# Kernel optimization log

Measured on AMD Instinct MI355X. Metric: run time of the kernel, lower is better.

Reference implementation:

```python
import jax, jax.numpy as jnp
import numpy as np

MARGIN = 1.0
BIG = 1e4  # larger than any cosine distance (max 2.0)

def setup_inputs() -> dict:
    key = jax.random.key(0)
    k1, k2 = jax.random.split(key)
    embeddings = jax.random.normal(k1, (4096, 512), dtype=jnp.float32)
    labels = jax.random.randint(k2, (4096,), 0, 512, dtype=jnp.int64)
    return {"embeddings": embeddings, "labels": labels}

def reference(embeddings, labels):
    b = embeddings.shape[0]
    # L2-normalize rows (torch F.normalize uses eps=1e-12 clamp on norm)
    norms = jnp.linalg.norm(embeddings, axis=1, keepdims=True)
    emb_n = embeddings / jnp.maximum(norms, 1e-12)
    sim = emb_n @ emb_n.T                      # [b, b]
    dist = jnp.maximum(1.0 - sim, 0.0)         # cosine distance, clamped at 0

    same = labels[:, None] == labels[None, :]  # [b, b]
    eye = jnp.eye(b, dtype=bool)
    pos_mask = same & ~eye
    neg_mask = ~same

    # batch-hard mining: row-wise masked max over positives, min over negatives
    hardest_pos = jnp.max(jnp.where(pos_mask, dist, 0.0), axis=1)   # dist >= 0 so 0 is neutral for max
    hardest_neg = jnp.min(jnp.where(neg_mask, dist, BIG), axis=1)

    valid = jnp.any(pos_mask, axis=1) & jnp.any(neg_mask, axis=1)
    per_row = jax.nn.relu(hardest_pos - hardest_neg + MARGIN)
    loss_sum = jnp.sum(jnp.where(valid, per_row, 0.0))
    num_valid = jnp.sum(valid)
    return loss_sum / jnp.maximum(num_valid, 1).astype(loss_sum.dtype)
```

## Files before the change

### kernel.cpp

```cpp
#include <hip/hip_runtime.h>
#include <hip/hip_bf16.h>

#define BATCH 4096
#define DIM   512
#define NLBL  512
#define BIGF  1e4f
#define MARGIN 1.0f

#define BM 128
#define BK 32
#define NT (BATCH/BM)
#define NPAIR (NT*(NT+1)/2)
#define KITERS (DIM/BK)

#define PANEL_E 4096
#define TILE_E  65536

using f32x4  = __attribute__((ext_vector_type(4))) float;
using bf16x8 = __attribute__((ext_vector_type(8))) short;

struct PairTab { unsigned char bi[NPAIR]; unsigned char bj[NPAIR]; };
constexpr PairTab make_tab() {
    PairTab t{};
    int idx = 0;
    for (int BI = 0; BI < 8; ++BI)
        for (int BJ = BI; BJ < 8; ++BJ)
            for (int ii = 0; ii < 4; ++ii)
                for (int jj = 0; jj < 4; ++jj) {
                    int i = BI * 4 + ii, j = BJ * 4 + jj;
                    if (i <= j) {
                        t.bi[idx] = (unsigned char)i;
                        t.bj[idx] = (unsigned char)j;
                        ++idx;
                    }
                }
    return t;
}
__device__ constexpr PairTab PT = make_tab();

__device__ __forceinline__ unsigned short f2bf(float x) {
    __hip_bfloat16 h = __float2bfloat16(x);
    return *reinterpret_cast<unsigned short*>(&h);
}

#define GLOAD16(gp, lp) \
    __builtin_amdgcn_global_load_lds((const __attribute__((address_space(1))) void*)(gp), \
                                     (__attribute__((address_space(3))) void*)(lp), 16, 0, 0)

__global__ __launch_bounds__(256) void normalize_k(const float* __restrict__ emb,
                                                   unsigned short* __restrict__ HiT,
                                                   unsigned* __restrict__ hp,
                                                   unsigned* __restrict__ hn) {
    int wave = threadIdx.x >> 6;
    int lane = threadIdx.x & 63;
    int row  = blockIdx.x * 4 + wave;
    const float4* src = (const float4*)(emb + (size_t)row * DIM);
    float4 v0 = src[lane * 2];
    float4 v1 = src[lane * 2 + 1];
    float ss = v0.x*v0.x + v0.y*v0.y + v0.z*v0.z + v0.w*v0.w
             + v1.x*v1.x + v1.y*v1.y + v1.z*v1.z + v1.w*v1.w;
    #pragma unroll
    for (int off = 1; off < 64; off <<= 1) ss += __shfl_xor(ss, off);
    float scale = 1.0f / fmaxf(sqrtf(ss), 1e-12f);
    bf16x8 o;
    o[0] = (short)f2bf(v0.x * scale);
    o[1] = (short)f2bf(v0.y * scale);
    o[2] = (short)f2bf(v0.z * scale);
    o[3] = (short)f2bf(v0.w * scale);
    o[4] = (short)f2bf(v1.x * scale);
    o[5] = (short)f2bf(v1.y * scale);
    o[6] = (short)f2bf(v1.z * scale);
    o[7] = (short)f2bf(v1.w * scale);
    size_t off = (size_t)(row >> 7) * TILE_E + (size_t)(lane >> 2) * PANEL_E
               + (size_t)(row & 127) * 32 + (lane & 3) * 8;
    *(bf16x8*)(HiT + off) = o;
    if (lane == 0) {
        hp[row] = 0u;
        hn[row] = __float_as_uint(BIGF);
    }
}

__global__ __launch_bounds__(256, 4) void mine_k(const unsigned short* __restrict__ HiT,
                                                 const int* __restrict__ lab,
                                                 unsigned* __restrict__ hp,
                                                 unsigned* __restrict__ hn) {
    __shared__ __attribute__((aligned(16))) unsigned short As[2][BM * BK];
    __shared__ __attribute__((aligned(16))) unsigned short Bs[2][BM * BK];
    __shared__ float rowp[2][BM], rown[2][BM], colp[2][BM], coln[2][BM];

    int orig = (int)blockIdx.x;
    int p = (orig & 7) * (NPAIR / 8) + (orig >> 3);
    const int bi = PT.bi[p];
    const int bj = PT.bj[p];
    const int i0 = bi * BM;
    const int j0 = bj * BM;

    const int tid  = threadIdx.x;
    const int w    = tid >> 6;
    const int lane = tid & 63;
    const int wr   = w >> 1;
    const int wc   = w & 1;
    const int l15  = lane & 15;
    const int lhi  = lane >> 4;

    f32x4 acc[4][4] = {};
    const char* HiB = (const char*)HiT;

    auto STAGE = [&](int buf, int t) {
        const size_t pa = ((size_t)bi * 16 + t) * (PANEL_E * 2);
        const size_t pb = ((size_t)bj * 16 + t) * (PANEL_E * 2);
        const int rrel = lane >> 2;
        #pragma unroll
        for (int q = 0; q < 2; ++q) {
            const int R   = w * 32 + q * 16 + rrel;
            const int sc  = (lane & 3) ^ ((R >> 1) & 3);
            const int soff = (w * 2048 + q * 1024) + rrel * 64 + (sc << 4);
            GLOAD16(HiB + pa + soff, (char*)As[buf] + (w * 32 + q * 16) * 64);
            GLOAD16(HiB + pb + soff, (char*)Bs[buf] + (w * 32 + q * 16) * 64);
        }
    };
    auto COMPUTE = [&](int buf) {
        bf16x8 a[4], b[4];
        #pragma unroll
        for (int m = 0; m < 4; ++m) {
            int row = wr * 64 + m * 16 + l15;
            int cp  = lhi ^ ((row >> 1) & 3);
            a[m] = *(const bf16x8*)((const char*)As[buf] + row * 64 + (cp << 4));
        }
        #pragma unroll
        for (int n = 0; n < 4; ++n) {
            int row = wc * 64 + n * 16 + l15;
            int cp  = lhi ^ ((row >> 1) & 3);
            b[n] = *(const bf16x8*)((const char*)Bs[buf] + row * 64 + (cp << 4));
        }
        #pragma unroll
        for (int m = 0; m < 4; ++m)
            #pragma unroll
            for (int n = 0; n < 4; ++n)
                acc[m][n] = __builtin_amdgcn_mfma_f32_16x16x32_bf16(a[m], b[n], acc[m][n], 0, 0, 0);
    };

    STAGE(0, 0);
    STAGE(1, 1);
    #pragma unroll
    for (int t = 0; t < KITERS; ++t) {
        const int cur = t & 1;
        if (t < KITERS - 1) {
            asm volatile("s_waitcnt vmcnt(4)" ::: "memory");
        } else {
            asm volatile("s_waitcnt vmcnt(0)" ::: "memory");
        }
        __builtin_amdgcn_sched_barrier(0);
        __builtin_amdgcn_s_barrier();
        COMPUTE(cur);
        __builtin_amdgcn_sched_barrier(0);
        __builtin_amdgcn_s_barrier();
        if (t + 2 < KITERS) STAGE(cur, t + 2);
    }

    int lj[4];
    #pragma unroll
    for (int n = 0; n < 4; ++n) lj[n] = lab[j0 + wc * 64 + n * 16 + l15];
    int li[16];
    #pragma unroll
    for (int m = 0; m < 4; ++m)
        #pragma unroll
        for (int r = 0; r < 4; ++r)
            li[m * 4 + r] = lab[i0 + wr * 64 + m * 16 + lhi * 4 + r];

    #pragma unroll
    for (int m = 0; m < 4; ++m) {
        #pragma unroll
        for (int r = 0; r < 4; ++r) {
            int i   = i0 + wr * 64 + m * 16 + lhi * 4 + r;
            int lir = li[m * 4 + r];
            float pm = 0.0f, nm = BIGF;
            #pragma unroll
            for (int n = 0; n < 4; ++n) {
                float dist = fmaxf(1.0f - acc[m][n][r], 0.0f);
                int j = j0 + wc * 64 + n * 16 + l15;
                if (lir == lj[n]) {
                    if (i != j) pm = fmaxf(pm, dist);
                } else {
                    nm = fminf(nm, dist);
                }
            }
            #pragma unroll
            for (int off = 1; off < 16; off <<= 1) {
                pm = fmaxf(pm, __shfl_xor(pm, off));
                nm = fminf(nm, __shfl_xor(nm, off));
            }
            if (l15 == 0) {
                int loc = wr * 64 + m * 16 + lhi * 4 + r;
                rowp[wc][loc] = pm;
                rown[wc][loc] = nm;
            }
        }
    }

    #pragma unroll
    for (int n = 0; n < 4; ++n) {
        int j   = j0 + wc * 64 + n * 16 + l15;
        int ljn = lj[n];
        float cp = 0.0f, cn = BIGF;
        #pragma unroll
        for (int m = 0; m < 4; ++m) {
            #pragma unroll
            for (int r = 0; r < 4; ++r) {
                float dist = fmaxf(1.0f - acc[m][n][r], 0.0f);
                int i = i0 + wr * 64 + m * 16 + lhi * 4 + r;
                if (li[m * 4 + r] == ljn) {
                    if (i != j) cp = fmaxf(cp, dist);
                } else {
                    cn = fminf(cn, dist);
                }
            }
        }
        #pragma unroll
        for (int off = 16; off < 64; off <<= 1) {
            cp = fmaxf(cp, __shfl_xor(cp, off));
            cn = fminf(cn, __shfl_xor(cn, off));
        }
        if (lhi == 0) {
            int loc = wc * 64 + n * 16 + l15;
            colp[wr][loc] = cp;
            coln[wr][loc] = cn;
        }
    }

    __syncthreads();

    if (tid < BM) {
        float pmv = fmaxf(rowp[0][tid], rowp[1][tid]);
        float nmv = fminf(rown[0][tid], rown[1][tid]);
        atomicMax(hp + i0 + tid, __float_as_uint(pmv));
        atomicMin(hn + i0 + tid, __float_as_uint(nmv));
    } else {
        int c = tid - BM;
        float pmv = fmaxf(colp[0][c], colp[1][c]);
        float nmv = fminf(coln[0][c], coln[1][c]);
        atomicMax(hp + j0 + c, __float_as_uint(pmv));
        atomicMin(hn + j0 + c, __float_as_uint(nmv));
    }
}

__global__ __launch_bounds__(1024) void final_k(const int* __restrict__ lab,
                                                const unsigned* __restrict__ hp,
                                                const unsigned* __restrict__ hn,
                                                float* __restrict__ out) {
    __shared__ int   cnt[NLBL];
    __shared__ float ssum[16];
    __shared__ int   scnt[16];
    int t = threadIdx.x;
    for (int i = t; i < NLBL; i += 1024) cnt[i] = 0;
    __syncthreads();
    for (int i = t; i < BATCH; i += 1024) atomicAdd(&cnt[lab[i]], 1);
    __syncthreads();

    float lsum = 0.0f;
    int   lcnt = 0;
    for (int i = t; i < BATCH; i += 1024) {
        int c = cnt[lab[i]];
        if ((c > 1) && (c < BATCH)) {
            float per = fmaxf(__uint_as_float(hp[i]) - __uint_as_float(hn[i]) + MARGIN, 0.0f);
            lsum += per;
            lcnt += 1;
        }
    }
    #pragma unroll
    for (int off = 1; off < 64; off <<= 1) {
        lsum += __shfl_xor(lsum, off);
        lcnt += __shfl_xor(lcnt, off);
    }
    int w = t >> 6;
    if ((t & 63) == 0) { ssum[w] = lsum; scnt[w] = lcnt; }
    __syncthreads();
    if (t == 0) {
        float s = 0.0f; int c2 = 0;
        #pragma unroll
        for (int i = 0; i < 16; ++i) { s += ssum[i]; c2 += scnt[i]; }
        out[0] = s / (float)max(c2, 1);
    }
}

extern "C" void kernel_launch(void* const* d_in, const int* in_sizes, int n_in,
                              void* d_out, int out_size, void* d_ws, size_t ws_size,
                              hipStream_t stream) {
    const float* emb = (const float*)d_in[0];
    const int*   lab = (const int*)d_in[1];

    char* base = (char*)d_ws;
    unsigned short* HiT = (unsigned short*)base;
    unsigned* hp = (unsigned*)(base + (size_t)BATCH * DIM * 2);
    unsigned* hn = hp + BATCH;

    normalize_k<<<BATCH / 4, 256, 0, stream>>>(emb, HiT, hp, hn);
    mine_k<<<NPAIR, 256, 0, stream>>>(HiT, lab, hp, hn);
    final_k<<<1, 1024, 0, stream>>>(lab, hp, hn, (float*)d_out);
}
```

Baseline: 35.51 us.

## Enlarge mining tiles to 256x256 with 512 threads and triple-buffered loads

```diff
diff --git a/kernel.cpp b/kernel.cpp
--- a/kernel.cpp
+++ b/kernel.cpp
@@ -7,7 +7,7 @@
 #define BIGF  1e4f
 #define MARGIN 1.0f
 
-#define BM 128
+#define BM 256
 #define BK 32
 #define NT (BATCH/BM)
 #define NPAIR (NT*(NT+1)/2)
@@ -23,17 +23,12 @@
 constexpr PairTab make_tab() {
     PairTab t{};
     int idx = 0;
-    for (int BI = 0; BI < 8; ++BI)
-        for (int BJ = BI; BJ < 8; ++BJ)
-            for (int ii = 0; ii < 4; ++ii)
-                for (int jj = 0; jj < 4; ++jj) {
-                    int i = BI * 4 + ii, j = BJ * 4 + jj;
-                    if (i <= j) {
-                        t.bi[idx] = (unsigned char)i;
-                        t.bj[idx] = (unsigned char)j;
-                        ++idx;
-                    }
-                }
+    for (int i = 0; i < NT; ++i)
+        for (int j = i; j < NT; ++j) {
+            t.bi[idx] = (unsigned char)i;
+            t.bj[idx] = (unsigned char)j;
+            ++idx;
+        }
     return t;
 }
 __device__ constexpr PairTab PT = make_tab();
@@ -80,13 +75,14 @@
     }
 }
 
-__global__ __launch_bounds__(256, 4) void mine_k(const unsigned short* __restrict__ HiT,
+__global__ __launch_bounds__(512, 2) void mine_k(const unsigned short* __restrict__ HiT,
                                                  const int* __restrict__ lab,
                                                  unsigned* __restrict__ hp,
                                                  unsigned* __restrict__ hn) {
-    __shared__ __attribute__((aligned(16))) unsigned short As[2][BM * BK];
-    __shared__ __attribute__((aligned(16))) unsigned short Bs[2][BM * BK];
-    __shared__ float rowp[2][BM], rown[2][BM], colp[2][BM], coln[2][BM];
+    __shared__ __attribute__((aligned(16))) unsigned short As[3][BM * BK];
+    __shared__ __attribute__((aligned(16))) unsigned short Bs[3][BM * BK];
+    __shared__ float rowp[4][BM], rown[4][BM];
+    __shared__ float colp[2][BM], coln[2][BM];
 
     int orig = (int)blockIdx.x;
     int p = (orig & 7) * (NPAIR / 8) + (orig >> 3);
@@ -98,32 +94,33 @@
     const int tid  = threadIdx.x;
     const int w    = tid >> 6;
     const int lane = tid & 63;
-    const int wr   = w >> 1;
-    const int wc   = w & 1;
+    const int wr   = w >> 2;
+    const int wc   = w & 3;
     const int l15  = lane & 15;
     const int lhi  = lane >> 4;
 
-    f32x4 acc[4][4] = {};
+    f32x4 acc[8][4] = {};
     const char* HiB = (const char*)HiT;
 
     auto STAGE = [&](int buf, int t) {
-        const size_t pa = ((size_t)bi * 16 + t) * (PANEL_E * 2);
-        const size_t pb = ((size_t)bj * 16 + t) * (PANEL_E * 2);
         const int rrel = lane >> 2;
         #pragma unroll
-        for (int q = 0; q < 2; ++q) {
-            const int R   = w * 32 + q * 16 + rrel;
-            const int sc  = (lane & 3) ^ ((R >> 1) & 3);
-            const int soff = (w * 2048 + q * 1024) + rrel * 64 + (sc << 4);
-            GLOAD16(HiB + pa + soff, (char*)As[buf] + (w * 32 + q * 16) * 64);
-            GLOAD16(HiB + pb + soff, (char*)Bs[buf] + (w * 32 + q * 16) * 64);
+        for (int s = 0; s < 2; ++s) {
+            const int r16 = (w * 2 + s) * 16;
+            const int rowl = r16 + rrel;
+            const int sc  = (lane & 3) ^ ((rowl >> 1) & 3);
+            const size_t pa = ((size_t)((i0 >> 7) * 16 + (r16 >> 7) * 16 + t)) * (PANEL_E * 2);
+            const size_t pb = ((size_t)((j0 >> 7) * 16 + (r16 >> 7) * 16 + t)) * (PANEL_E * 2);
+            const int soff = ((rowl & 127)) * 64 + (sc << 4);
+            GLOAD16(HiB + pa + soff, (char*)As[buf] + r16 * 64);
+            GLOAD16(HiB + pb + soff, (char*)Bs[buf] + r16 * 64);
         }
     };
     auto COMPUTE = [&](int buf) {
-        bf16x8 a[4], b[4];
-        #pragma unroll
-        for (int m = 0; m < 4; ++m) {
-            int row = wr * 64 + m * 16 + l15;
+        bf16x8 a[8], b[4];
+        #pragma unroll
+        for (int m = 0; m < 8; ++m) {
+            int row = wr * 128 + m * 16 + l15;
             int cp  = lhi ^ ((row >> 1) & 3);
             a[m] = *(const bf16x8*)((const char*)As[buf] + row * 64 + (cp << 4));
         }
@@ -134,7 +131,7 @@
             b[n] = *(const bf16x8*)((const char*)Bs[buf] + row * 64 + (cp << 4));
         }
         #pragma unroll
-        for (int m = 0; m < 4; ++m)
+        for (int m = 0; m < 8; ++m)
             #pragma unroll
             for (int n = 0; n < 4; ++n)
                 acc[m][n] = __builtin_amdgcn_mfma_f32_16x16x32_bf16(a[m], b[n], acc[m][n], 0, 0, 0);
@@ -142,10 +139,13 @@
 
     STAGE(0, 0);
     STAGE(1, 1);
+    STAGE(2, 2);
     #pragma unroll
     for (int t = 0; t < KITERS; ++t) {
-        const int cur = t & 1;
-        if (t < KITERS - 1) {
+        const int cur = t % 3;
+        if (t <= KITERS - 3) {
+            asm volatile("s_waitcnt vmcnt(8)" ::: "memory");
+        } else if (t == KITERS - 2) {
             asm volatile("s_waitcnt vmcnt(4)" ::: "memory");
         } else {
             asm volatile("s_waitcnt vmcnt(0)" ::: "memory");
@@ -155,24 +155,24 @@
         COMPUTE(cur);
         __builtin_amdgcn_sched_barrier(0);
         __builtin_amdgcn_s_barrier();
-        if (t + 2 < KITERS) STAGE(cur, t + 2);
+        if (t + 3 < KITERS) STAGE(cur, t + 3);
     }
 
     int lj[4];
     #pragma unroll
     for (int n = 0; n < 4; ++n) lj[n] = lab[j0 + wc * 64 + n * 16 + l15];
-    int li[16];
-    #pragma unroll
-    for (int m = 0; m < 4; ++m)
+    int li[32];
+    #pragma unroll
+    for (int m = 0; m < 8; ++m)
         #pragma unroll
         for (int r = 0; r < 4; ++r)
-            li[m * 4 + r] = lab[i0 + wr * 64 + m * 16 + lhi * 4 + r];
-
-    #pragma unroll
-    for (int m = 0; m < 4; ++m) {
+            li[m * 4 + r] = lab[i0 + wr * 128 + m * 16 + lhi * 4 + r];
+
+    #pragma unroll
+    for (int m = 0; m < 8; ++m) {
         #pragma unroll
         for (int r = 0; r < 4; ++r) {
-            int i   = i0 + wr * 64 + m * 16 + lhi * 4 + r;
+            int i   = i0 + wr * 128 + m * 16 + lhi * 4 + r;
             int lir = li[m * 4 + r];
             float pm = 0.0f, nm = BIGF;
             #pragma unroll
@@ -191,7 +191,7 @@
                 nm = fminf(nm, __shfl_xor(nm, off));
             }
             if (l15 == 0) {
-                int loc = wr * 64 + m * 16 + lhi * 4 + r;
+                int loc = wr * 128 + m * 16 + lhi * 4 + r;
                 rowp[wc][loc] = pm;
                 rown[wc][loc] = nm;
             }
@@ -204,11 +204,11 @@
         int ljn = lj[n];
         float cp = 0.0f, cn = BIGF;
         #pragma unroll
-        for (int m = 0; m < 4; ++m) {
+        for (int m = 0; m < 8; ++m) {
             #pragma unroll
             for (int r = 0; r < 4; ++r) {
                 float dist = fmaxf(1.0f - acc[m][n][r], 0.0f);
-                int i = i0 + wr * 64 + m * 16 + lhi * 4 + r;
+                int i = i0 + wr * 128 + m * 16 + lhi * 4 + r;
                 if (li[m * 4 + r] == ljn) {
                     if (i != j) cp = fmaxf(cp, dist);
                 } else {
@@ -231,8 +231,8 @@
     __syncthreads();
 
     if (tid < BM) {
-        float pmv = fmaxf(rowp[0][tid], rowp[1][tid]);
-        float nmv = fminf(rown[0][tid], rown[1][tid]);
+        float pmv = fmaxf(fmaxf(rowp[0][tid], rowp[1][tid]), fmaxf(rowp[2][tid], rowp[3][tid]));
+        float nmv = fminf(fminf(rown[0][tid], rown[1][tid]), fminf(rown[2][tid], rown[3][tid]));
         atomicMax(hp + i0 + tid, __float_as_uint(pmv));
         atomicMin(hn + i0 + tid, __float_as_uint(nmv));
     } else {
@@ -295,6 +295,6 @@
     unsigned* hn = hp + BATCH;
 
     normalize_k<<<BATCH / 4, 256, 0, stream>>>(emb, HiT, hp, hn);
-    mine_k<<<NPAIR, 256, 0, stream>>>(HiT, lab, hp, hn);
+    mine_k<<<NPAIR, 512, 0, stream>>>(HiT, lab, hp, hn);
     final_k<<<1, 1024, 0, stream>>>(lab, hp, hn, (float*)d_out);
 }
```

Result: slower. 46.99 us (+32.3%).

## Switch similarity GEMM from bf16 to fp8 MFMA with halved operand storage

Applied to the files above, without the earlier changes.

```diff
diff --git a/kernel.cpp b/kernel.cpp
--- a/kernel.cpp
+++ b/kernel.cpp
@@ -8,16 +8,14 @@
 #define MARGIN 1.0f
 
 #define BM 128
-#define BK 32
+#define BK 64
 #define NT (BATCH/BM)
 #define NPAIR (NT*(NT+1)/2)
 #define KITERS (DIM/BK)
 
-#define PANEL_E 4096
-#define TILE_E  65536
+#define PANEL_B 8192
 
 using f32x4  = __attribute__((ext_vector_type(4))) float;
-using bf16x8 = __attribute__((ext_vector_type(8))) short;
 
 struct PairTab { unsigned char bi[NPAIR]; unsigned char bj[NPAIR]; };
 constexpr PairTab make_tab() {
@@ -38,17 +36,12 @@
 }
 __device__ constexpr PairTab PT = make_tab();
 
-__device__ __forceinline__ unsigned short f2bf(float x) {
-    __hip_bfloat16 h = __float2bfloat16(x);
-    return *reinterpret_cast<unsigned short*>(&h);
-}
-
 #define GLOAD16(gp, lp) \
     __builtin_amdgcn_global_load_lds((const __attribute__((address_space(1))) void*)(gp), \
                                      (__attribute__((address_space(3))) void*)(lp), 16, 0, 0)
 
 __global__ __launch_bounds__(256) void normalize_k(const float* __restrict__ emb,
-                                                   unsigned short* __restrict__ HiT,
+                                                   unsigned char* __restrict__ Hi8,
                                                    unsigned* __restrict__ hp,
                                                    unsigned* __restrict__ hn) {
     int wave = threadIdx.x >> 6;
@@ -62,30 +55,27 @@
     #pragma unroll
     for (int off = 1; off < 64; off <<= 1) ss += __shfl_xor(ss, off);
     float scale = 1.0f / fmaxf(sqrtf(ss), 1e-12f);
-    bf16x8 o;
-    o[0] = (short)f2bf(v0.x * scale);
-    o[1] = (short)f2bf(v0.y * scale);
-    o[2] = (short)f2bf(v0.z * scale);
-    o[3] = (short)f2bf(v0.w * scale);
-    o[4] = (short)f2bf(v1.x * scale);
-    o[5] = (short)f2bf(v1.y * scale);
-    o[6] = (short)f2bf(v1.z * scale);
-    o[7] = (short)f2bf(v1.w * scale);
-    size_t off = (size_t)(row >> 7) * TILE_E + (size_t)(lane >> 2) * PANEL_E
-               + (size_t)(row & 127) * 32 + (lane & 3) * 8;
-    *(bf16x8*)(HiT + off) = o;
+    int w0 = 0, w1 = 0;
+    w0 = __builtin_amdgcn_cvt_pk_fp8_f32(v0.x * scale, v0.y * scale, w0, false);
+    w0 = __builtin_amdgcn_cvt_pk_fp8_f32(v0.z * scale, v0.w * scale, w0, true);
+    w1 = __builtin_amdgcn_cvt_pk_fp8_f32(v1.x * scale, v1.y * scale, w1, false);
+    w1 = __builtin_amdgcn_cvt_pk_fp8_f32(v1.z * scale, v1.w * scale, w1, true);
+    size_t off = ((size_t)(row >> 7) * 8 + (lane >> 3)) * PANEL_B
+               + (size_t)(row & 127) * 64 + (lane & 7) * 8;
+    int2 o; o.x = w0; o.y = w1;
+    *(int2*)(Hi8 + off) = o;
     if (lane == 0) {
         hp[row] = 0u;
         hn[row] = __float_as_uint(BIGF);
     }
 }
 
-__global__ __launch_bounds__(256, 4) void mine_k(const unsigned short* __restrict__ HiT,
+__global__ __launch_bounds__(256, 4) void mine_k(const unsigned char* __restrict__ Hi8,
                                                  const int* __restrict__ lab,
                                                  unsigned* __restrict__ hp,
                                                  unsigned* __restrict__ hn) {
-    __shared__ __attribute__((aligned(16))) unsigned short As[2][BM * BK];
-    __shared__ __attribute__((aligned(16))) unsigned short Bs[2][BM * BK];
+    __shared__ __attribute__((aligned(16))) unsigned char As[2][BM * BK];
+    __shared__ __attribute__((aligned(16))) unsigned char Bs[2][BM * BK];
     __shared__ float rowp[2][BM], rown[2][BM], colp[2][BM], coln[2][BM];
 
     int orig = (int)blockIdx.x;
@@ -104,40 +94,43 @@
     const int lhi  = lane >> 4;
 
     f32x4 acc[4][4] = {};
-    const char* HiB = (const char*)HiT;
+    const char* HiB = (const char*)Hi8;
 
     auto STAGE = [&](int buf, int t) {
-        const size_t pa = ((size_t)bi * 16 + t) * (PANEL_E * 2);
-        const size_t pb = ((size_t)bj * 16 + t) * (PANEL_E * 2);
+        const size_t pa = ((size_t)bi * 8 + t) * PANEL_B;
+        const size_t pb = ((size_t)bj * 8 + t) * PANEL_B;
         const int rrel = lane >> 2;
         #pragma unroll
         for (int q = 0; q < 2; ++q) {
-            const int R   = w * 32 + q * 16 + rrel;
-            const int sc  = (lane & 3) ^ ((R >> 1) & 3);
-            const int soff = (w * 2048 + q * 1024) + rrel * 64 + (sc << 4);
+            const int r   = w * 32 + q * 16 + rrel;
+            const int c16 = (lane & 3) ^ ((r >> 1) & 3);
+            const int soff = r * 64 + (c16 << 4);
             GLOAD16(HiB + pa + soff, (char*)As[buf] + (w * 32 + q * 16) * 64);
             GLOAD16(HiB + pb + soff, (char*)Bs[buf] + (w * 32 + q * 16) * 64);
         }
     };
     auto COMPUTE = [&](int buf) {
-        bf16x8 a[4], b[4];
-        #pragma unroll
-        for (int m = 0; m < 4; ++m) {
-            int row = wr * 64 + m * 16 + l15;
-            int cp  = lhi ^ ((row >> 1) & 3);
-            a[m] = *(const bf16x8*)((const char*)As[buf] + row * 64 + (cp << 4));
-        }
-        #pragma unroll
-        for (int n = 0; n < 4; ++n) {
-            int row = wc * 64 + n * 16 + l15;
-            int cp  = lhi ^ ((row >> 1) & 3);
-            b[n] = *(const bf16x8*)((const char*)Bs[buf] + row * 64 + (cp << 4));
-        }
-        #pragma unroll
-        for (int m = 0; m < 4; ++m)
-            #pragma unroll
-            for (int n = 0; n < 4; ++n)
-                acc[m][n] = __builtin_amdgcn_mfma_f32_16x16x32_bf16(a[m], b[n], acc[m][n], 0, 0, 0);
+        #pragma unroll
+        for (int kk = 0; kk < 2; ++kk) {
+            long a[4], b[4];
+            #pragma unroll
+            for (int m = 0; m < 4; ++m) {
+                int row = wr * 64 + m * 16 + l15;
+                int cp  = (kk * 2 + (lhi >> 1)) ^ ((row >> 1) & 3);
+                a[m] = *(const long*)((const char*)As[buf] + row * 64 + (cp << 4) + (lhi & 1) * 8);
+            }
+            #pragma unroll
+            for (int n = 0; n < 4; ++n) {
+                int row = wc * 64 + n * 16 + l15;
+                int cp  = (kk * 2 + (lhi >> 1)) ^ ((row >> 1) & 3);
+                b[n] = *(const long*)((const char*)Bs[buf] + row * 64 + (cp << 4) + (lhi & 1) * 8);
+            }
+            #pragma unroll
+            for (int m = 0; m < 4; ++m)
+                #pragma unroll
+                for (int n = 0; n < 4; ++n)
+                    acc[m][n] = __builtin_amdgcn_mfma_f32_16x16x32_fp8_fp8(a[m], b[n], acc[m][n], 0, 0, 0);
+        }
     };
 
     STAGE(0, 0);
@@ -290,11 +283,11 @@
     const int*   lab = (const int*)d_in[1];
 
     char* base = (char*)d_ws;
-    unsigned short* HiT = (unsigned short*)base;
-    unsigned* hp = (unsigned*)(base + (size_t)BATCH * DIM * 2);
+    unsigned char* Hi8 = (unsigned char*)base;
+    unsigned* hp = (unsigned*)(base + (size_t)BATCH * DIM);
     unsigned* hn = hp + BATCH;
 
-    normalize_k<<<BATCH / 4, 256, 0, stream>>>(emb, HiT, hp, hn);
-    mine_k<<<NPAIR, 256, 0, stream>>>(HiT, lab, hp, hn);
+    normalize_k<<<BATCH / 4, 256, 0, stream>>>(emb, Hi8, hp, hn);
+    mine_k<<<NPAIR, 256, 0, stream>>>(Hi8, lab, hp, hn);
     final_k<<<1, 1024, 0, stream>>>(lab, hp, hn, (float*)d_out);
 }
```

New measurement: 32.33 us. -9.0%, faster.
